# Kernel optimization log

Hardware: AMD Instinct MI355X
Metric: run time of the kernel (lower is better)

The kernel has to match this reference:

```python
import jax, jax.numpy as jnp
import numpy as np

MID = 64      # mid_channels
KSQ = 9       # kernel_size**2

def setup_inputs() -> dict:
    key = jax.random.key(0)
    k1, k2 = jax.random.split(key, 2)
    x = jax.random.normal(k1, (8, 256, 128, 128), dtype=jnp.float32)
    # 1x1 conv weight [out_c=640, in_c=256]; fan-in scaled init like torch Conv2d
    W = jax.random.normal(k2, (MID * (1 + KSQ), 256), dtype=jnp.float32) * (1.0 / np.sqrt(256.0))
    b = jnp.zeros((MID * (1 + KSQ),), dtype=jnp.float32)
    return {"x": x, "W": W, "b": b}

def reference(x, W, b):
    B, C, H, Wd = x.shape
    # 1x1 conv == channel contraction
    raw = jnp.einsum('bchw,oc->bohw', x, W) + b[None, :, None, None]   # [B, 640, H, W]
    score_map = raw[:, :MID]                                           # [B, MID, H, W]
    kernel_map = raw[:, MID:].reshape(B, MID, KSQ, H, Wd)              # [B, MID, 9, H, W]
    # adaptive_avg_pool2d(.,1) -> mean over HW, then sigmoid
    global_scores = jax.nn.sigmoid(score_map.mean(axis=(2, 3)))        # [B, MID]
    norm_kernels = jax.nn.softmax(kernel_map, axis=2)                  # softmax over 9-tap kernel dim
    # eval mode: scale from current global scores, clamped
    scale = jnp.clip(global_scores.mean(), 0.25, 1.0)
    k = int(np.ceil(MID * float(scale)))
    k = max(k, max(4, MID // 4))
    # topk channel selection per sample
    _, idx_full = jax.lax.top_k(global_scores, MID)
    indices = idx_full[:, :k]                                          # [B, k]
    # scatter ones into mask
    mask = jnp.zeros_like(global_scores).at[jnp.arange(B)[:, None], indices].set(1.0)
    mask = mask[:, :, None, None]                                      # [B, MID, 1, 1]
    return (mask, norm_kernels, k, indices)
```

## Files before the change

kernel.cpp:

```cpp
#include <hip/hip_runtime.h>
#include <math.h>

constexpr int CIN      = 256;
constexpr int HW       = 16384;
constexpr int NMID     = 64;
constexpr int HWTILE   = 128;
constexpr int TILE_B   = 8192;
constexpr int NORM_OFF = 512;
constexpr int K_OFF    = 75497984;
constexpr int IDX_OFF  = 75497985;

typedef __attribute__((ext_vector_type(8))) short bf16x8;
typedef __attribute__((ext_vector_type(4))) float f32x4;

__device__ __forceinline__ unsigned bf16_rne(float f) {
    unsigned u = __float_as_uint(f);
    return (u + 0x7fffu + ((u >> 16) & 1u)) >> 16;
}

__global__ __launch_bounds__(256) void prep_w(const float* __restrict__ Wm,
                                              char* __restrict__ ws)
{
    const int o = blockIdx.x;
    const int c = threadIdx.x;
    int mid, j;
    if (o < NMID) { mid = o; j = 0; }
    else          { mid = (o - NMID) / 9; j = 1 + (o - NMID) % 9; }
    const int g  = mid >> 3, ml = mid & 7, q = ml >> 1, mi = ml & 1;
    const int idx = mi * 10 + j;
    const int p   = (idx >> 2) * 16 + q * 4 + (idx & 3);
    const float w = Wm[(size_t)o * CIN + c];
    const unsigned hi = bf16_rne(w);
    const float    fl = w - __uint_as_float(hi << 16);
    const unsigned lo = bf16_rne(fl);
    const int kc = c >> 5, cc = c & 31;
    char* base = ws + (size_t)((g * 8 + kc) * 2) * TILE_B + p * 80 + cc * 2;
    *(unsigned short*)(base)          = (unsigned short)hi;
    *(unsigned short*)(base + TILE_B) = (unsigned short)lo;
}

__global__ __launch_bounds__(512) void zero_mask_kernel(float* __restrict__ out) {
    out[threadIdx.x] = 0.0f;
}

__global__ __launch_bounds__(256, 2) void fused_main(const float* __restrict__ x,
                                                     const char* __restrict__ wimg,
                                                     const float* __restrict__ bvec,
                                                     float* __restrict__ out)
{
    const int tid  = threadIdx.x;
    const int wave = tid >> 6, lane = tid & 63;
    const int q    = lane >> 4, m = lane & 15;
    const int b    = blockIdx.x >> 7;
    const int hw0  = (blockIdx.x & 127) * HWTILE;
    const int grot = (blockIdx.x >> 3) & 7;

    bf16x8 Bhi[2][8], Blo[2][8];
    const float* xb = x + (size_t)b * CIN * HW + hw0 + wave * 32 + m;
    #pragma unroll
    for (int t = 0; t < 2; ++t)
        #pragma unroll
        for (int kc = 0; kc < 8; ++kc) {
            float f[8];
            #pragma unroll
            for (int i = 0; i < 8; ++i)
                f[i] = xb[t * 16 + (size_t)(kc * 32 + q * 8 + i) * HW];
            union { unsigned u[4]; bf16x8 v; } uh, ul;
            #pragma unroll
            for (int jj = 0; jj < 4; ++jj) {
                const unsigned h0 = bf16_rne(f[2*jj]), h1 = bf16_rne(f[2*jj+1]);
                const float r0 = f[2*jj]   - __uint_as_float(h0 << 16);
                const float r1 = f[2*jj+1] - __uint_as_float(h1 << 16);
                uh.u[jj] = h0 | (h1 << 16);
                ul.u[jj] = bf16_rne(r0) | (bf16_rne(r1) << 16);
            }
            Bhi[t][kc] = uh.v; Blo[t][kc] = ul.v;
        }

    const char* aptr = wimg + m * 80 + q * 16;
    const float* bv9 = bvec + NMID;

    #pragma unroll 1
    for (int gg = 0; gg < 8; ++gg) {
        const int g = (gg + grot) & 7;
        f32x4 acc[5][2];
        #pragma unroll
        for (int ot = 0; ot < 5; ++ot)
            #pragma unroll
            for (int t = 0; t < 2; ++t) acc[ot][t] = (f32x4){0.f, 0.f, 0.f, 0.f};

        #pragma unroll
        for (int kc = 0; kc < 8; ++kc) {
            const char* ap = aptr + (size_t)((g * 8 + kc) * 2) * TILE_B;
            bf16x8 Ah[5], Al[5];
            #pragma unroll
            for (int ot = 0; ot < 5; ++ot) {
                Ah[ot] = *(const bf16x8*)(ap + ot * 1280);
                Al[ot] = *(const bf16x8*)(ap + TILE_B + ot * 1280);
            }
            __builtin_amdgcn_s_setprio(1);
            #pragma unroll
            for (int ot = 0; ot < 5; ++ot)
                #pragma unroll
                for (int t2 = 0; t2 < 2; ++t2)
                    acc[ot][t2] = __builtin_amdgcn_mfma_f32_16x16x32_bf16(Ah[ot], Bhi[t2][kc], acc[ot][t2], 0, 0, 0);
            #pragma unroll
            for (int ot = 0; ot < 5; ++ot)
                #pragma unroll
                for (int t2 = 0; t2 < 2; ++t2)
                    acc[ot][t2] = __builtin_amdgcn_mfma_f32_16x16x32_bf16(Ah[ot], Blo[t2][kc], acc[ot][t2], 0, 0, 0);
            #pragma unroll
            for (int ot = 0; ot < 5; ++ot)
                #pragma unroll
                for (int t2 = 0; t2 < 2; ++t2)
                    acc[ot][t2] = __builtin_amdgcn_mfma_f32_16x16x32_bf16(Al[ot], Bhi[t2][kc], acc[ot][t2], 0, 0, 0);
            __builtin_amdgcn_s_setprio(0);
        }

        #pragma unroll
        for (int mi = 0; mi < 2; ++mi) {
            const int gmid = g * 8 + q * 2 + mi;
            const int i0 = mi * 10;
            float s = acc[i0 >> 2][0][i0 & 3] + acc[i0 >> 2][1][i0 & 3];
            s += __shfl_xor(s, 1); s += __shfl_xor(s, 2);
            s += __shfl_xor(s, 4); s += __shfl_xor(s, 8);
            if (m == 0) atomicAdd(&out[b * NMID + gmid], s);
            float bj[9];
            #pragma unroll
            for (int jj = 0; jj < 9; ++jj) bj[jj] = bv9[gmid * 9 + jj];
            #pragma unroll
            for (int t2 = 0; t2 < 2; ++t2) {
                float p[9];
                #pragma unroll
                for (int jj = 0; jj < 9; ++jj) {
                    const int idx = i0 + 1 + jj;
                    p[jj] = acc[idx >> 2][t2][idx & 3] + bj[jj];
                }
                float mx = p[0];
                #pragma unroll
                for (int jj = 1; jj < 9; ++jj) mx = fmaxf(mx, p[jj]);
                float ss = 0.f;
                #pragma unroll
                for (int jj = 0; jj < 9; ++jj) { p[jj] = __expf(p[jj] - mx); ss += p[jj]; }
                const float rs = 1.0f / ss;
                float* ob = out + NORM_OFF
                          + ((size_t)((b * NMID + gmid) * 9)) * HW
                          + hw0 + wave * 32 + t2 * 16 + m;
                #pragma unroll
                for (int jj = 0; jj < 9; ++jj)
                    __builtin_nontemporal_store(p[jj] * rs, ob + (size_t)jj * HW);
            }
        }
    }
}

__global__ __launch_bounds__(512) void finalize_kernel(float* __restrict__ out,
                                                       const float* __restrict__ bvec,
                                                       int k)
{
    const int tid  = threadIdx.x;
    const int b    = tid >> 6;
    const int lane = tid & 63;
    const float sum = out[b * NMID + lane];
    const float sv  = 1.0f / (1.0f + __expf(-(sum * (1.0f / 16384.0f) + bvec[lane])));
    float val      = sv;
    float selected = 0.0f;
    for (int t = 0; t < k; ++t) {
        float bvv = val;
        int   bi  = lane;
        #pragma unroll
        for (int off = 32; off >= 1; off >>= 1) {
            const float ov = __shfl_xor(bvv, off);
            const int   oi = __shfl_xor(bi, off);
            if (ov > bvv || (ov == bvv && oi < bi)) { bvv = ov; bi = oi; }
        }
        if (lane == bi) { val = -INFINITY; selected = 1.0f; }
        if (lane == 0) out[IDX_OFF + b * k + t] = (float)bi;
    }
    out[b * NMID + lane] = selected;
    if (tid == 0) out[K_OFF] = (float)k;
}

extern "C" void kernel_launch(void* const* d_in, const int* in_sizes, int n_in,
                              void* d_out, int out_size, void* d_ws, size_t ws_size,
                              hipStream_t stream)
{
    const float* x    = (const float*)d_in[0];
    const float* Wm   = (const float*)d_in[1];
    const float* bvec = (const float*)d_in[2];
    float* out = (float*)d_out;
    char*  ws  = (char*)d_ws;

    const int k = (out_size - IDX_OFF) / 8;

    prep_w<<<640, 256, 0, stream>>>(Wm, ws);
    zero_mask_kernel<<<1, 512, 0, stream>>>(out);
    fused_main<<<8 * (HW / HWTILE), 256, 0, stream>>>(x, ws, bvec, out);
    finalize_kernel<<<1, 512, 0, stream>>>(out, bvec, k);
}
```

Baseline: 195.6 us.

## Stage weight tiles into LDS with triple-buffered async global_load_lds pipeline

Instead of every wave loading its weight fragments straight from global memory, the block now copies each 16 KB hi/lo weight tile into a three-deep LDS ring using global_load_lds, prefetching two tiles ahead. Hand-tuned vmcnt waits and barriers order these copies against the MFMA loop, and the epilogue moves inside the k-loop so the vmcnt counts cover the output stores. Bias values are also staged in LDS. The aim is to cut redundant per-wave global and L2 weight traffic and to hide its latency. In exchange it adds about 50 KB of LDS, which can limit occupancy, plus two barriers per k-step, and it relies on fragile hardcoded wait counts.

```diff
diff --git a/kernel.cpp b/kernel.cpp
--- a/kernel.cpp
+++ b/kernel.cpp
@@ -16,6 +16,12 @@
 __device__ __forceinline__ unsigned bf16_rne(float f) {
     unsigned u = __float_as_uint(f);
     return (u + 0x7fffu + ((u >> 16) & 1u)) >> 16;
+}
+
+__device__ __forceinline__ void gload_lds16(const void* gsrc, void* ldst) {
+    __builtin_amdgcn_global_load_lds(
+        (const __attribute__((address_space(1))) void*)gsrc,
+        (__attribute__((address_space(3))) void*)ldst, 16, 0, 0);
 }
 
 __global__ __launch_bounds__(256) void prep_w(const float* __restrict__ Wm,
@@ -48,6 +54,9 @@
                                                      const float* __restrict__ bvec,
                                                      float* __restrict__ out)
 {
+    __shared__ __align__(16) char atile[3][2][TILE_B];
+    __shared__ float bsh[576];
+
     const int tid  = threadIdx.x;
     const int wave = tid >> 6, lane = tid & 63;
     const int q    = lane >> 4, m = lane & 15;
@@ -55,6 +64,19 @@
     const int hw0  = (blockIdx.x & 127) * HWTILE;
     const int grot = (blockIdx.x >> 3) & 7;
 
+#define STAGE(tile, buf) do {                                                  \
+    const char* _s = wimg + (size_t)(tile) * 2 * TILE_B;                       \
+    char* _d = &atile[buf][0][0];                                              \
+    gload_lds16(_s + tid * 16,                 _d + tid * 16);                 \
+    gload_lds16(_s + 4096 + tid * 16,          _d + 4096 + tid * 16);          \
+    gload_lds16(_s + TILE_B + tid * 16,        _d + TILE_B + tid * 16);        \
+    gload_lds16(_s + TILE_B + 4096 + tid * 16, _d + TILE_B + 4096 + tid * 16); \
+} while (0)
+
+    const int t0 = grot * 8;
+    STAGE(t0, 0);
+    STAGE(t0 + 1, 1);
+
     bf16x8 Bhi[2][8], Blo[2][8];
     const float* xb = x + (size_t)b * CIN * HW + hw0 + wave * 32 + m;
     #pragma unroll
@@ -76,10 +98,11 @@
             }
             Bhi[t][kc] = uh.v; Blo[t][kc] = ul.v;
         }
-
-    const char* aptr = wimg + m * 80 + q * 16;
-    const float* bv9 = bvec + NMID;
-
+    for (int i = tid; i < 576; i += 256) bsh[i] = bvec[NMID + i];
+    asm volatile("s_waitcnt lgkmcnt(0)" ::: "memory");
+    __builtin_amdgcn_s_barrier();
+
+    int cur = 0;
     #pragma unroll 1
     for (int gg = 0; gg < 8; ++gg) {
         const int g = (gg + grot) & 7;
@@ -91,12 +114,25 @@
 
         #pragma unroll
         for (int kc = 0; kc < 8; ++kc) {
-            const char* ap = aptr + (size_t)((g * 8 + kc) * 2) * TILE_B;
+            const int seq = gg * 8 + kc;
+            const int nb  = (cur >= 1) ? cur - 1 : 2;
+            if (seq <= 61) {
+                const int nseq = seq + 2;
+                STAGE((((nseq >> 3) + grot) & 7) * 8 + (nseq & 7), nb);
+            }
+            if (gg == 7 && kc == 7)      asm volatile("s_waitcnt vmcnt(0)"  ::: "memory");
+            else if (gg == 7 && kc == 6) asm volatile("s_waitcnt vmcnt(4)"  ::: "memory");
+            else if (gg > 0 && kc < 2)   asm volatile("s_waitcnt vmcnt(46)" ::: "memory");
+            else                         asm volatile("s_waitcnt vmcnt(8)"  ::: "memory");
+            __builtin_amdgcn_s_barrier();
+
+            const char* ahi = &atile[cur][0][m * 80 + q * 16];
+            const char* alo = &atile[cur][1][m * 80 + q * 16];
             bf16x8 Ah[5], Al[5];
             #pragma unroll
             for (int ot = 0; ot < 5; ++ot) {
-                Ah[ot] = *(const bf16x8*)(ap + ot * 1280);
-                Al[ot] = *(const bf16x8*)(ap + TILE_B + ot * 1280);
+                Ah[ot] = *(const bf16x8*)(ahi + ot * 1280);
+                Al[ot] = *(const bf16x8*)(alo + ot * 1280);
             }
             __builtin_amdgcn_s_setprio(1);
             #pragma unroll
@@ -115,43 +151,49 @@
                 for (int t2 = 0; t2 < 2; ++t2)
                     acc[ot][t2] = __builtin_amdgcn_mfma_f32_16x16x32_bf16(Al[ot], Bhi[t2][kc], acc[ot][t2], 0, 0, 0);
             __builtin_amdgcn_s_setprio(0);
-        }
-
-        #pragma unroll
-        for (int mi = 0; mi < 2; ++mi) {
-            const int gmid = g * 8 + q * 2 + mi;
-            const int i0 = mi * 10;
-            float s = acc[i0 >> 2][0][i0 & 3] + acc[i0 >> 2][1][i0 & 3];
-            s += __shfl_xor(s, 1); s += __shfl_xor(s, 2);
-            s += __shfl_xor(s, 4); s += __shfl_xor(s, 8);
-            if (m == 0) atomicAdd(&out[b * NMID + gmid], s);
-            float bj[9];
-            #pragma unroll
-            for (int jj = 0; jj < 9; ++jj) bj[jj] = bv9[gmid * 9 + jj];
-            #pragma unroll
-            for (int t2 = 0; t2 < 2; ++t2) {
-                float p[9];
-                #pragma unroll
-                for (int jj = 0; jj < 9; ++jj) {
-                    const int idx = i0 + 1 + jj;
-                    p[jj] = acc[idx >> 2][t2][idx & 3] + bj[jj];
+
+            if (kc == 7) {
+                #pragma unroll
+                for (int mi = 0; mi < 2; ++mi) {
+                    const int gmid = g * 8 + q * 2 + mi;
+                    const int i0 = mi * 10;
+                    float s = acc[i0 >> 2][0][i0 & 3] + acc[i0 >> 2][1][i0 & 3];
+                    s += __shfl_xor(s, 1); s += __shfl_xor(s, 2);
+                    s += __shfl_xor(s, 4); s += __shfl_xor(s, 8);
+                    if (m == 0) atomicAdd(&out[b * NMID + gmid], s);
+                    float bj[9];
+                    #pragma unroll
+                    for (int jj = 0; jj < 9; ++jj) bj[jj] = bsh[gmid * 9 + jj];
+                    #pragma unroll
+                    for (int t2 = 0; t2 < 2; ++t2) {
+                        float p[9];
+                        #pragma unroll
+                        for (int jj = 0; jj < 9; ++jj) {
+                            const int idx = i0 + 1 + jj;
+                            p[jj] = acc[idx >> 2][t2][idx & 3] + bj[jj];
+                        }
+                        float mx = p[0];
+                        #pragma unroll
+                        for (int jj = 1; jj < 9; ++jj) mx = fmaxf(mx, p[jj]);
+                        float ss = 0.f;
+                        #pragma unroll
+                        for (int jj = 0; jj < 9; ++jj) { p[jj] = __expf(p[jj] - mx); ss += p[jj]; }
+                        const float rs = 1.0f / ss;
+                        float* ob = out + NORM_OFF
+                                  + ((size_t)((b * NMID + gmid) * 9)) * HW
+                                  + hw0 + wave * 32 + t2 * 16 + m;
+                        #pragma unroll
+                        for (int jj = 0; jj < 9; ++jj)
+                            __builtin_nontemporal_store(p[jj] * rs, ob + (size_t)jj * HW);
+                    }
                 }
-                float mx = p[0];
-                #pragma unroll
-                for (int jj = 1; jj < 9; ++jj) mx = fmaxf(mx, p[jj]);
-                float ss = 0.f;
-                #pragma unroll
-                for (int jj = 0; jj < 9; ++jj) { p[jj] = __expf(p[jj] - mx); ss += p[jj]; }
-                const float rs = 1.0f / ss;
-                float* ob = out + NORM_OFF
-                          + ((size_t)((b * NMID + gmid) * 9)) * HW
-                          + hw0 + wave * 32 + t2 * 16 + m;
-                #pragma unroll
-                for (int jj = 0; jj < 9; ++jj)
-                    __builtin_nontemporal_store(p[jj] * rs, ob + (size_t)jj * HW);
-            }
+            }
+            asm volatile("s_waitcnt lgkmcnt(0)" ::: "memory");
+            __builtin_amdgcn_s_barrier();
+            cur = (cur == 2) ? 0 : cur + 1;
         }
     }
+#undef STAGE
 }
 
 __global__ __launch_bounds__(512) void finalize_kernel(float* __restrict__ out,
```

Measured after the change: 181.9 us. 1.08x faster.
